# Optimization experiments

Measured on AMD Instinct MI355X. Metric: run time of the kernel, lower is better.

Reference implementation:

```python
import jax, jax.numpy as jnp
import numpy as np

D_MODEL = 1024
N_HEAD = 16
HEAD_D = D_MODEL // N_HEAD
D_FF = 4096
LN_EPS = 1e-5
ATTN_EPS = 1e-6


def _layer_norm(x, g, b, eps=LN_EPS):
    mu = jnp.mean(x, axis=-1, keepdims=True)
    var = jnp.var(x, axis=-1, keepdims=True)
    return (x - mu) * jax.lax.rsqrt(var + eps) * g + b


def setup_inputs() -> dict:
    key = jax.random.key(0)
    ks = jax.random.split(key, 16)
    s = 0.02
    return {
        "src": jax.random.normal(ks[0], (4, 4096, D_MODEL), dtype=jnp.float32),
        "qkv_w": jax.random.normal(ks[1], (D_MODEL, 3 * D_MODEL), dtype=jnp.float32) * s,
        "qkv_b": jax.random.normal(ks[2], (3 * D_MODEL,), dtype=jnp.float32) * s,
        "out_w": jax.random.normal(ks[3], (D_MODEL, D_MODEL), dtype=jnp.float32) * s,
        "out_b": jax.random.normal(ks[4], (D_MODEL,), dtype=jnp.float32) * s,
        "w1": jax.random.normal(ks[5], (D_MODEL, D_FF), dtype=jnp.float32) * s,
        "b1": jax.random.normal(ks[6], (D_FF,), dtype=jnp.float32) * s,
        "w2": jax.random.normal(ks[7], (D_FF, D_MODEL), dtype=jnp.float32) * s,
        "b2": jax.random.normal(ks[8], (D_MODEL,), dtype=jnp.float32) * s,
        "g1": jnp.ones((D_MODEL,), dtype=jnp.float32),
        "be1": jnp.zeros((D_MODEL,), dtype=jnp.float32),
        "g2": jnp.ones((D_MODEL,), dtype=jnp.float32),
        "be2": jnp.zeros((D_MODEL,), dtype=jnp.float32),
    }


def _linear_attention(x, qkv_w, qkv_b, out_w, out_b):
    B, N, C = x.shape
    qkv = (x @ qkv_w + qkv_b).reshape(B, N, 3, N_HEAD, HEAD_D)
    qkv = jnp.transpose(qkv, (2, 0, 3, 1, 4))  # [3,B,H,N,D]
    q, k, v = qkv[0], qkv[1], qkv[2]
    # phi = elu(x) + 1 (positive feature map)
    qf = jax.nn.elu(q) + 1.0
    kf = jax.nn.elu(k) + 1.0
    # kv aggregation: [B,H,D,D]
    kv = jnp.einsum('bhnd,bhne->bhde', kf.astype(jnp.float32), v.astype(jnp.float32)).astype(v.dtype)
    y_num = jnp.einsum('bhnd,bhde->bhne', qf, kv)  # [B,H,N,D]
    z = jnp.sum(kf.astype(jnp.float32), axis=2)  # [B,H,D]
    y_den = jnp.einsum('bhnd,bhd->bhn', qf, z.astype(qf.dtype))
    y_den = jnp.maximum(y_den, ATTN_EPS)[..., None]
    y = (y_num / y_den).transpose(0, 2, 1, 3).reshape(B, N, C)
    return y @ out_w + out_b


def reference(src, qkv_w, qkv_b, out_w, out_b, w1, b1, w2, b2, g1, be1, g2, be2):
    # pre-norm (norm_first=True), dropout disabled (eval)
    attn_out = _linear_attention(_layer_norm(src, g1, be1), qkv_w, qkv_b, out_w, out_b)
    x = src + attn_out
    h = jax.nn.gelu(_layer_norm(x, g2, be2) @ w1 + b1, approximate=False)
    return x + h @ w2 + b2
```

## Files before the change

### kernel.cpp

```cpp
#include <hip/hip_runtime.h>
#include <hip/hip_bf16.h>
#include <math.h>

typedef __attribute__((ext_vector_type(8))) short short8;
typedef __attribute__((ext_vector_type(4))) float floatx4;

__device__ __forceinline__ float bf2f(unsigned int u) {
    union { unsigned int i; float f; } c; c.i = u << 16; return c.f;
}
__device__ __forceinline__ unsigned short f2bf(float f) {
    unsigned int x = __builtin_bit_cast(unsigned int, f);
    unsigned int r = (x + 0x7fffu + ((x >> 16) & 1u)) >> 16;
    return (unsigned short)r;
}
__device__ __forceinline__ float elu1(float x) { return x > 0.f ? x + 1.f : __expf(x); }
__device__ __forceinline__ float gelu_fast(float x) {
    float u = x * (1.f + 0.044715f * x * x);
    return x / (1.f + __expf(-1.5957691216f * u));
}

__device__ __forceinline__ void async_cp16(const void* g, void* l) {
    __builtin_amdgcn_global_load_lds(
        (const __attribute__((address_space(1))) unsigned int*)g,
        (__attribute__((address_space(3))) unsigned int*)l, 16, 0, 0);
}

__global__ void prep_kernel(const float* __restrict__ qkv_w, const float* __restrict__ out_w,
                            const float* __restrict__ w1, const float* __restrict__ w2,
                            unsigned short* __restrict__ qkvwT, unsigned short* __restrict__ outwT,
                            unsigned short* __restrict__ w1T, unsigned short* __restrict__ w2T,
                            float* __restrict__ kvz) {
    const int bid = blockIdx.x;
    const int tx = threadIdx.x, ty = threadIdx.y;
    if (bid >= 12288) {
        const int lid = ty * 32 + tx;
        const int i = (bid - 12288) * 1024 + lid * 4;
        *(float4*)(kvz + i) = make_float4(0.f, 0.f, 0.f, 0.f);
        return;
    }
    const float* in;
    unsigned short* op;
    int K, N, tb;
    if (bid < 3072)      { in = qkv_w; op = qkvwT; K = 1024; N = 3072; tb = bid; }
    else if (bid < 4096) { in = out_w; op = outwT; K = 1024; N = 1024; tb = bid - 3072; }
    else if (bid < 8192) { in = w1;    op = w1T;   K = 1024; N = 4096; tb = bid - 4096; }
    else                 { in = w2;    op = w2T;   K = 4096; N = 1024; tb = bid - 8192; }
    const int nx = N >> 5;
    const int n0 = (tb % nx) * 32, k0 = (tb / nx) * 32;
    __shared__ float tile[32][33];
#pragma unroll
    for (int i = 0; i < 4; i++)
        tile[ty + 8 * i][tx] = in[(size_t)(k0 + ty + 8 * i) * N + n0 + tx];
    __syncthreads();
#pragma unroll
    for (int i = 0; i < 4; i++)
        op[(size_t)(n0 + ty + 8 * i) * K + k0 + tx] = f2bf(tile[tx][ty + 8 * i]);
}

template <int IN_BF16>
__global__ __launch_bounds__(256)
void ln_kernel(const void* __restrict__ xv, const float* __restrict__ g,
               const float* __restrict__ be, unsigned short* __restrict__ out) {
    const int row = blockIdx.x;
    const int t = threadIdx.x;
    float4 v;
    if (IN_BF16) {
        const unsigned short* x = (const unsigned short*)xv;
        uint2 r = *(const uint2*)(x + (size_t)row * 1024 + t * 4);
        v.x = bf2f(r.x & 0xffff); v.y = bf2f(r.x >> 16);
        v.z = bf2f(r.y & 0xffff); v.w = bf2f(r.y >> 16);
    } else {
        v = *(const float4*)((const float*)xv + (size_t)row * 1024 + t * 4);
    }
    float s = v.x + v.y + v.z + v.w;
    float s2 = v.x * v.x + v.y * v.y + v.z * v.z + v.w * v.w;
#pragma unroll
    for (int off = 32; off > 0; off >>= 1) {
        s += __shfl_down(s, off);
        s2 += __shfl_down(s2, off);
    }
    __shared__ float red[8];
    __shared__ float stat[2];
    const int w = t >> 6, l = t & 63;
    if (l == 0) { red[w] = s; red[4 + w] = s2; }
    __syncthreads();
    if (t == 0) {
        float S = red[0] + red[1] + red[2] + red[3];
        float S2 = red[4] + red[5] + red[6] + red[7];
        float mu = S * (1.f / 1024.f);
        float var = S2 * (1.f / 1024.f) - mu * mu;
        stat[0] = mu;
        stat[1] = rsqrtf(var + 1e-5f);
    }
    __syncthreads();
    const float mu = stat[0], rs = stat[1];
    const float4 gv = *(const float4*)(g + t * 4);
    const float4 bv = *(const float4*)(be + t * 4);
    unsigned int o0 = f2bf((v.x - mu) * rs * gv.x + bv.x);
    unsigned int o1 = f2bf((v.y - mu) * rs * gv.y + bv.y);
    unsigned int o2 = f2bf((v.z - mu) * rs * gv.z + bv.z);
    unsigned int o3 = f2bf((v.w - mu) * rs * gv.w + bv.w);
    uint2 pk;
    pk.x = o0 | (o1 << 16);
    pk.y = o2 | (o3 << 16);
    *(uint2*)(out + (size_t)row * 1024 + t * 4) = pk;
}

template <int EPI>
__global__ __launch_bounds__(256, 4)
void gemm_bt(const unsigned short* __restrict__ A, const unsigned short* __restrict__ B,
             const float* __restrict__ bias, const float* __restrict__ resid,
             const unsigned short* __restrict__ residb,
             unsigned short* __restrict__ Cbf, float* __restrict__ Cf32,
             int N, int K) {
    __shared__ unsigned short At[128 * 32];
    __shared__ unsigned short Bt[128 * 32];
    const int t = threadIdx.x;
    const int l = t & 63;
    const int w = t >> 6;

    const int T = gridDim.x * gridDim.y;
    const int f = blockIdx.y * gridDim.x + blockIdx.x;
    int bx = blockIdx.x, by = blockIdx.y;
    if ((T & 7) == 0) {
        const int per = T >> 3;
        const int g = (f & 7) * per + (f >> 3);
        bx = g % gridDim.x;
        by = g / gridDim.x;
    }
    const int m0 = by * 128;
    const int n0 = bx * 128;
    const int wm = (w >> 1) * 64;
    const int wn = (w & 1) * 64;

    floatx4 acc[4][4];
    const floatx4 zz = {0.f, 0.f, 0.f, 0.f};
#pragma unroll
    for (int i = 0; i < 4; i++)
#pragma unroll
        for (int j = 0; j < 4; j++) acc[i][j] = zz;

    const int sr = t >> 2;
    const int sc = (((t & 3) ^ ((t >> 3) & 3)) << 3);
    const unsigned short* ag = A + (size_t)(m0 + sr) * K + sc;
    const unsigned short* ag2 = ag + (size_t)64 * K;
    const unsigned short* bg = B + (size_t)(n0 + sr) * K + sc;
    const unsigned short* bg2 = bg + (size_t)64 * K;
    unsigned short* la = At + t * 8;
    unsigned short* la2 = At + 2048 + t * 8;
    unsigned short* lb = Bt + t * 8;
    unsigned short* lb2 = Bt + 2048 + t * 8;

    const int fr = l & 15;
    const int fo = (((l >> 4) ^ ((l >> 1) & 3)) << 3);

    for (int k0 = 0; k0 < K; k0 += 32) {
        async_cp16(ag + k0, la);
        async_cp16(ag2 + k0, la2);
        async_cp16(bg + k0, lb);
        async_cp16(bg2 + k0, lb2);
        __syncthreads();
        short8 af[4], bf[4];
#pragma unroll
        for (int i = 0; i < 4; i++)
            af[i] = *(const short8*)(At + (wm + i * 16 + fr) * 32 + fo);
#pragma unroll
        for (int i = 0; i < 4; i++)
            bf[i] = *(const short8*)(Bt + (wn + i * 16 + fr) * 32 + fo);
#pragma unroll
        for (int i = 0; i < 4; i++)
#pragma unroll
            for (int j = 0; j < 4; j++)
                acc[i][j] = __builtin_amdgcn_mfma_f32_16x16x32_bf16(af[i], bf[j], acc[i][j], 0, 0, 0);
        __syncthreads();
    }

    const int er = (l >> 4) << 2;
    const int ec = l & 15;
#pragma unroll
    for (int j = 0; j < 4; j++) {
        const int col = n0 + wn + j * 16 + ec;
        const float bb = bias[col];
#pragma unroll
        for (int i = 0; i < 4; i++) {
            const int rowb = m0 + wm + i * 16 + er;
#pragma unroll
            for (int r = 0; r < 4; r++) {
                const int row = rowb + r;
                float v = acc[i][j][r] + bb;
                const size_t idx = (size_t)row * N + col;
                if (EPI == 0) {
                    if (col < 2048) v = elu1(v);
                    Cbf[idx] = f2bf(v);
                } else if (EPI == 2) {
                    Cbf[idx] = f2bf(gelu_fast(v));
                } else if (EPI == 3) {
                    Cbf[idx] = f2bf(v + resid[idx]);
                } else {
                    Cf32[idx] = v + bf2f(residb[idx]);
                }
            }
        }
    }
}

__global__ __launch_bounds__(256)
void kv_kernel(const unsigned short* __restrict__ qkv, float* __restrict__ kvz) {
    const int bh = blockIdx.x;
    const int chunk = blockIdx.y;
    const int b = bh >> 4, h = bh & 15;
    const int t = threadIdx.x;
    __shared__ float kf[64][68];
    __shared__ float vv[64][68];
    const int te = t >> 4, td = t & 15;
    float acc[4][4];
#pragma unroll
    for (int i = 0; i < 4; i++)
#pragma unroll
        for (int j = 0; j < 4; j++) acc[i][j] = 0.f;
    float zacc = 0.f;
    const size_t base = (size_t)b * 4096 * 3072 + (size_t)chunk * 512 * 3072;
    const int koff = 1024 + h * 64;
    const int voff = 2048 + h * 64;
    const int rl = t >> 3, seg = t & 7;

    for (int s = 0; s < 8; s++) {
#pragma unroll
        for (int p = 0; p < 2; p++) {
            const int nl = p * 32 + rl;
            const unsigned short* rp = qkv + base + (size_t)(s * 64 + nl) * 3072;
            const uint4 kd = *(const uint4*)(rp + koff + seg * 8);
            const uint4 vd = *(const uint4*)(rp + voff + seg * 8);
            float* kdst = &kf[nl][seg * 8];
            float* vdst = &vv[nl][seg * 8];
            kdst[0] = bf2f(kd.x & 0xffff); kdst[1] = bf2f(kd.x >> 16);
            kdst[2] = bf2f(kd.y & 0xffff); kdst[3] = bf2f(kd.y >> 16);
            kdst[4] = bf2f(kd.z & 0xffff); kdst[5] = bf2f(kd.z >> 16);
            kdst[6] = bf2f(kd.w & 0xffff); kdst[7] = bf2f(kd.w >> 16);
            vdst[0] = bf2f(vd.x & 0xffff); vdst[1] = bf2f(vd.x >> 16);
            vdst[2] = bf2f(vd.y & 0xffff); vdst[3] = bf2f(vd.y >> 16);
            vdst[4] = bf2f(vd.z & 0xffff); vdst[5] = bf2f(vd.z >> 16);
            vdst[6] = bf2f(vd.w & 0xffff); vdst[7] = bf2f(vd.w >> 16);
        }
        __syncthreads();
        for (int n = 0; n < 64; n++) {
            const float4 kk = *(const float4*)&kf[n][te * 4];
            const float4 vn = *(const float4*)&vv[n][td * 4];
            const float ka[4] = {kk.x, kk.y, kk.z, kk.w};
            const float va[4] = {vn.x, vn.y, vn.z, vn.w};
#pragma unroll
            for (int i = 0; i < 4; i++)
#pragma unroll
                for (int j = 0; j < 4; j++) acc[i][j] = fmaf(ka[i], va[j], acc[i][j]);
        }
        if (t < 64) {
            for (int n = 0; n < 64; n++) zacc += kf[n][t];
        }
        __syncthreads();
    }
    float* kvp = kvz + bh * 4160;
#pragma unroll
    for (int i = 0; i < 4; i++)
#pragma unroll
        for (int j = 0; j < 4; j++)
            atomicAdd(&kvp[(te * 4 + i) * 64 + td * 4 + j], acc[i][j]);
    if (t < 64) atomicAdd(&kvp[4096 + t], zacc);
}

__global__ __launch_bounds__(256)
void y_kernel(const unsigned short* __restrict__ qkv, const float* __restrict__ kvz,
              unsigned short* __restrict__ y) {
    const int bh = blockIdx.x, chunk = blockIdx.y;
    const int b = bh >> 4, h = bh & 15;
    const int t = threadIdx.x;
    __shared__ float kv[64][68];
    __shared__ float zs[64];
    __shared__ float qf[16][68];
    const float* kvp = kvz + bh * 4160;
#pragma unroll
    for (int p = 0; p < 4; p++) {
        const int f = (t + p * 256) * 4;
        const float4 v4 = *(const float4*)(kvp + f);
        *(float4*)&kv[f >> 6][f & 63] = v4;
    }
    if (t < 16) *(float4*)&zs[t * 4] = *(const float4*)(kvp + 4096 + t * 4);
    __syncthreads();
    const int nl = t >> 4, td = t & 15;
    const size_t base = (size_t)b * 4096 * 3072 + (size_t)chunk * 128 * 3072;
    const int qoff = h * 64;
    for (int s = 0; s < 8; s++) {
        if (t < 128) {
            const int r = t >> 3, seg = t & 7;
            const uint4 qd = *(const uint4*)(qkv + base + (size_t)(s * 16 + r) * 3072 + qoff + seg * 8);
            float* qdst = &qf[r][seg * 8];
            qdst[0] = bf2f(qd.x & 0xffff); qdst[1] = bf2f(qd.x >> 16);
            qdst[2] = bf2f(qd.y & 0xffff); qdst[3] = bf2f(qd.y >> 16);
            qdst[4] = bf2f(qd.z & 0xffff); qdst[5] = bf2f(qd.z >> 16);
            qdst[6] = bf2f(qd.w & 0xffff); qdst[7] = bf2f(qd.w >> 16);
        }
        __syncthreads();
        float a0 = 0.f, a1 = 0.f, a2 = 0.f, a3 = 0.f, den = 0.f;
        for (int e = 0; e < 64; e++) {
            const float q = qf[nl][e];
            const float4 kvv = *(const float4*)&kv[e][td * 4];
            a0 = fmaf(q, kvv.x, a0);
            a1 = fmaf(q, kvv.y, a1);
            a2 = fmaf(q, kvv.z, a2);
            a3 = fmaf(q, kvv.w, a3);
            den = fmaf(q, zs[e], den);
        }
        const float inv = 1.f / fmaxf(den, 1e-6f);
        const int tok = b * 4096 + chunk * 128 + s * 16 + nl;
        unsigned int o0 = f2bf(a0 * inv), o1 = f2bf(a1 * inv);
        unsigned int o2 = f2bf(a2 * inv), o3 = f2bf(a3 * inv);
        uint2 pk;
        pk.x = o0 | (o1 << 16);
        pk.y = o2 | (o3 << 16);
        *(uint2*)(y + (size_t)tok * 1024 + h * 64 + td * 4) = pk;
        __syncthreads();
    }
}

extern "C" void kernel_launch(void* const* d_in, const int* in_sizes, int n_in,
                              void* d_out, int out_size, void* d_ws, size_t ws_size,
                              hipStream_t stream) {
    const float* src   = (const float*)d_in[0];
    const float* qkv_w = (const float*)d_in[1];
    const float* qkv_b = (const float*)d_in[2];
    const float* out_w = (const float*)d_in[3];
    const float* out_b = (const float*)d_in[4];
    const float* w1    = (const float*)d_in[5];
    const float* b1    = (const float*)d_in[6];
    const float* w2    = (const float*)d_in[7];
    const float* b2    = (const float*)d_in[8];
    const float* g1    = (const float*)d_in[9];
    const float* be1   = (const float*)d_in[10];
    const float* g2    = (const float*)d_in[11];
    const float* be2   = (const float*)d_in[12];
    float* outp = (float*)d_out;

    char* ws = (char*)d_ws;
    unsigned short* qkvwT = (unsigned short*)(ws + 0);
    unsigned short* outwT = (unsigned short*)(ws + 6291456);
    unsigned short* w1T   = (unsigned short*)(ws + 8388608);
    unsigned short* w2T   = (unsigned short*)(ws + 16777216);
    unsigned short* bufA  = (unsigned short*)(ws + 25165824);
    unsigned short* bufB  = (unsigned short*)(ws + 159383552);
    unsigned short* xbuf  = (unsigned short*)(ws + 192937984);
    float*          kvz   = (float*)(ws + 260046848);

    prep_kernel<<<12548, dim3(32, 8), 0, stream>>>(qkv_w, out_w, w1, w2,
                                                   qkvwT, outwT, w1T, w2T, kvz);

    ln_kernel<0><<<16384, 256, 0, stream>>>(src, g1, be1, bufB);
    gemm_bt<0><<<dim3(24, 128), 256, 0, stream>>>(bufB, qkvwT, qkv_b, nullptr, nullptr, bufA, nullptr, 3072, 1024);
    kv_kernel<<<dim3(64, 8), 256, 0, stream>>>(bufA, kvz);
    y_kernel<<<dim3(64, 32), 256, 0, stream>>>(bufA, kvz, bufB);
    gemm_bt<3><<<dim3(8, 128), 256, 0, stream>>>(bufB, outwT, out_b, src, nullptr, xbuf, nullptr, 1024, 1024);
    ln_kernel<1><<<16384, 256, 0, stream>>>(xbuf, g2, be2, bufB);
    gemm_bt<2><<<dim3(32, 128), 256, 0, stream>>>(bufB, w1T, b1, nullptr, nullptr, bufA, nullptr, 4096, 1024);
    gemm_bt<4><<<dim3(8, 128), 256, 0, stream>>>(bufA, w2T, b2, nullptr, xbuf, nullptr, outp, 1024, 4096);
}
```

Measured before the change: 847.0 us.

## Double GEMM K-tile to 64 with 8-way swizzle and XCD-aware block remap

The GEMM K-step grows from 32 to 64. Each iteration now issues eight async global-to-LDS copies per thread and runs two MFMA sub-steps between barriers, which halves the synchronisation count per K. The LDS swizzle becomes 8-way XOR to fit the 64-wide rows. The block-to-tile remap is changed for grids with 128 row-tiles so that each XCD gets a contiguous band of 16 row-tiles, walked in groups of 4 column-tiles, aiming at better L2 locality. LDS use doubles to 32KB per block, which may limit occupancy under launch_bounds(256,4).

```diff
diff --git a/kernel.cpp b/kernel.cpp
--- a/kernel.cpp
+++ b/kernel.cpp
@@ -113,20 +113,22 @@
              const unsigned short* __restrict__ residb,
              unsigned short* __restrict__ Cbf, float* __restrict__ Cf32,
              int N, int K) {
-    __shared__ unsigned short At[128 * 32];
-    __shared__ unsigned short Bt[128 * 32];
+    __shared__ unsigned short At[128 * 64];
+    __shared__ unsigned short Bt[128 * 64];
     const int t = threadIdx.x;
     const int l = t & 63;
     const int w = t >> 6;
 
-    const int T = gridDim.x * gridDim.y;
     const int f = blockIdx.y * gridDim.x + blockIdx.x;
     int bx = blockIdx.x, by = blockIdx.y;
-    if ((T & 7) == 0) {
-        const int per = T >> 3;
-        const int g = (f & 7) * per + (f >> 3);
-        bx = g % gridDim.x;
-        by = g / gridDim.x;
+    if (gridDim.y == 128 && (gridDim.x & 3) == 0) {
+        const int xcd = f & 7;
+        const int g = f >> 3;
+        const int nin = g & 3;
+        const int r = (g >> 2) & 15;
+        const int nchunk = g >> 6;
+        bx = nchunk * 4 + nin;
+        by = xcd * 16 + r;
     }
     const int m0 = by * 128;
     const int n0 = bx * 128;
@@ -140,38 +142,40 @@
 #pragma unroll
         for (int j = 0; j < 4; j++) acc[i][j] = zz;
 
-    const int sr = t >> 2;
-    const int sc = (((t & 3) ^ ((t >> 3) & 3)) << 3);
-    const unsigned short* ag = A + (size_t)(m0 + sr) * K + sc;
-    const unsigned short* ag2 = ag + (size_t)64 * K;
-    const unsigned short* bg = B + (size_t)(n0 + sr) * K + sc;
-    const unsigned short* bg2 = bg + (size_t)64 * K;
+    const int sr = t >> 3;
+    const int sg = ((t & 7) ^ ((t >> 3) & 7));
+    const unsigned short* ag = A + (size_t)(m0 + sr) * K + sg * 8;
+    const unsigned short* bg = B + (size_t)(n0 + sr) * K + sg * 8;
     unsigned short* la = At + t * 8;
-    unsigned short* la2 = At + 2048 + t * 8;
     unsigned short* lb = Bt + t * 8;
-    unsigned short* lb2 = Bt + 2048 + t * 8;
 
     const int fr = l & 15;
-    const int fo = (((l >> 4) ^ ((l >> 1) & 3)) << 3);
-
-    for (int k0 = 0; k0 < K; k0 += 32) {
-        async_cp16(ag + k0, la);
-        async_cp16(ag2 + k0, la2);
-        async_cp16(bg + k0, lb);
-        async_cp16(bg2 + k0, lb2);
-        __syncthreads();
-        short8 af[4], bf[4];
-#pragma unroll
-        for (int i = 0; i < 4; i++)
-            af[i] = *(const short8*)(At + (wm + i * 16 + fr) * 32 + fo);
-#pragma unroll
-        for (int i = 0; i < 4; i++)
-            bf[i] = *(const short8*)(Bt + (wn + i * 16 + fr) * 32 + fo);
-#pragma unroll
-        for (int i = 0; i < 4; i++)
-#pragma unroll
-            for (int j = 0; j < 4; j++)
-                acc[i][j] = __builtin_amdgcn_mfma_f32_16x16x32_bf16(af[i], bf[j], acc[i][j], 0, 0, 0);
+    const int fx = fr & 7;
+    const int g0 = (l >> 4);
+
+    for (int k0 = 0; k0 < K; k0 += 64) {
+#pragma unroll
+        for (int c = 0; c < 4; c++) {
+            async_cp16(ag + k0 + (size_t)(c * 32) * K, la + c * 2048);
+            async_cp16(bg + k0 + (size_t)(c * 32) * K, lb + c * 2048);
+        }
+        __syncthreads();
+#pragma unroll
+        for (int sub = 0; sub < 2; sub++) {
+            const int fo = ((sub * 4 + g0) ^ fx) << 3;
+            short8 af[4], bf[4];
+#pragma unroll
+            for (int i = 0; i < 4; i++)
+                af[i] = *(const short8*)(At + (wm + i * 16 + fr) * 64 + fo);
+#pragma unroll
+            for (int i = 0; i < 4; i++)
+                bf[i] = *(const short8*)(Bt + (wn + i * 16 + fr) * 64 + fo);
+#pragma unroll
+            for (int i = 0; i < 4; i++)
+#pragma unroll
+                for (int j = 0; j < 4; j++)
+                    acc[i][j] = __builtin_amdgcn_mfma_f32_16x16x32_bf16(af[i], bf[j], acc[i][j], 0, 0, 0);
+        }
         __syncthreads();
     }
 
```

After: 779.9 us. 7.9% less time.
